# Kernel optimization log

Hardware: AMD Instinct MI355X
Metric: run time of the kernel (lower is better)

Reference implementation:

```python
import jax, jax.numpy as jnp
import numpy as np

B, H, W = 8, 80, 160
N = B * H * W          # flattened pixels
G = 8                  # cost groups
D = 64                 # disparity candidates
NS = 4                 # num_seed
E = 128                # embed_dim
NFREQ = 15             # fourier freqs -> (2*15+1)*1 = 31 dims
NORMALIZER = 3.14 / 64


def setup_inputs() -> dict:
    key = jax.random.key(0)
    ks = jax.random.split(key, 8)
    cost_volume = jax.random.normal(ks[0], (N, G, D), jnp.float32)
    label_seed = jax.random.randint(ks[1], (N, NS), 0, D)
    context = jax.random.normal(ks[2], (B, H, W, E), jnp.float32)
    s = 0.02
    W1 = jax.random.normal(ks[3], (G * 9, E), jnp.float32) * s
    b1 = jnp.zeros((E,), jnp.float32)
    W2 = jax.random.normal(ks[4], (E, E), jnp.float32) * s
    b2 = jnp.zeros((E,), jnp.float32)
    Wp = jax.random.normal(ks[5], (E + 31, E), jnp.float32) * s
    return {"cost_volume": cost_volume, "label_seed": label_seed, "context": context,
            "W1": W1, "b1": b1, "W2": W2, "b2": b2, "Wp": Wp}


def sample_cost(cost_volume, label_seed):
    # cost_volume: [N,G,D], label_seed: [N,NS] -> [N,NS,G*9]
    offset = jnp.arange(-4, 5, dtype=label_seed.dtype)              # [9]
    idx = jnp.clip(label_seed[:, :, None] + offset, 0, D - 1)      # [N,NS,9]
    idx = jnp.broadcast_to(idx.reshape(N, 1, NS * 9), (N, G, NS * 9))
    cost = jnp.take_along_axis(cost_volume, idx, axis=-1)          # [N,G,NS*9]
    # rearrange 'b h (n c) -> b n (h c)'
    cost = cost.reshape(N, G, NS, 9).transpose(0, 2, 1, 3).reshape(N, NS, G * 9)
    return cost


def fourier_embed(label_f):
    # label_f: [N,NS] float -> [N,NS,31]
    coord = label_f * NORMALIZER                                   # [N,NS]
    freqs = 2.0 ** jnp.arange(NFREQ, dtype=label_f.dtype)          # logscale bands
    f = coord[..., None] * freqs                                   # [N,NS,15]
    return jnp.concatenate([jnp.sin(f), jnp.cos(f), coord[..., None]], axis=-1)


def reference(cost_volume, label_seed, context, W1, b1, W2, b2, Wp):
    cost = sample_cost(cost_volume, label_seed)                    # [N,NS,72]
    h = jax.nn.gelu(cost @ W1 + b1, approximate=False)
    cost_feat = h @ W2 + b2                                        # [N,NS,E]
    label_f = label_seed.astype(jnp.float32)
    disp_enc = fourier_embed(label_f)                              # [N,NS,31]
    sample_embed = jnp.concatenate([cost_feat, disp_enc], axis=-1) @ Wp  # [N,NS,E]
    # layers=[] and norm=None -> passthrough; context unused
    return sample_embed[None], label_f
```

## Files before the change

kernel.cpp:

```cpp
#include <hip/hip_runtime.h>
#include <hip/hip_bf16.h>
#include <math.h>

#define NPIX 102400
#define NSEED 4
#define RTOT (NPIX * NSEED)
#define GG 8
#define DD 64
#define EE 128
#define BM 64

#define KP1 96
#define KP2 128
#define KP3 160

#define PC 104
#define PH 136
#define PF 168

typedef short bf16x8 __attribute__((ext_vector_type(8)));
typedef short bf16x4 __attribute__((ext_vector_type(4)));
typedef float f32x4 __attribute__((ext_vector_type(4)));

static __device__ __forceinline__ short f2bf(float x) {
    __hip_bfloat16 h = __float2bfloat16(x);
    return __builtin_bit_cast(short, h);
}

static __device__ __forceinline__ float gelu_exact(float x) {
    return 0.5f * x * (1.0f + erff(x * 0.7071067811865475f));
}

__global__ void prep_weights(const float* __restrict__ W1,
                             const float* __restrict__ W2,
                             const float* __restrict__ Wp,
                             short* __restrict__ ws) {
    const int i = blockIdx.x * 256 + threadIdx.x;
    if (i < 12288) {
        const int e = i / KP1, k = i - e * KP1;
        ws[i] = (k < 72) ? f2bf(W1[k * EE + e]) : (short)0;
    } else if (i < 12288 + 16384) {
        const int j = i - 12288;
        const int e = j / KP2, k = j - e * KP2;
        ws[i] = f2bf(W2[k * EE + e]);
    } else if (i < 49152) {
        const int j = i - 28672;
        const int e = j / KP3, k = j - e * KP3;
        ws[i] = (k < 159) ? f2bf(Wp[k * EE + e]) : (short)0;
    }
}

template <int KPAD, int PADB>
__device__ __forceinline__ void gemm_tiles(const short* __restrict__ WT, const short* sB,
                                           int mt0, int ln, int qd, f32x4 acc[2][4]) {
#pragma unroll
    for (int ks = 0; ks < KPAD / 32; ++ks) {
        const int kb = ks * 32 + qd * 8;
        const bf16x8 a0 = *(const bf16x8*)(WT + (mt0 * 16 + ln) * KPAD + kb);
        const bf16x8 a1 = *(const bf16x8*)(WT + (mt0 * 16 + 16 + ln) * KPAD + kb);
        const bf16x8 b0 = *(const bf16x8*)(sB + (0 * 16 + ln) * PADB + kb);
        const bf16x8 b1 = *(const bf16x8*)(sB + (1 * 16 + ln) * PADB + kb);
        const bf16x8 b2 = *(const bf16x8*)(sB + (2 * 16 + ln) * PADB + kb);
        const bf16x8 b3 = *(const bf16x8*)(sB + (3 * 16 + ln) * PADB + kb);
        acc[0][0] = __builtin_amdgcn_mfma_f32_16x16x32_bf16(a0, b0, acc[0][0], 0, 0, 0);
        acc[0][1] = __builtin_amdgcn_mfma_f32_16x16x32_bf16(a0, b1, acc[0][1], 0, 0, 0);
        acc[0][2] = __builtin_amdgcn_mfma_f32_16x16x32_bf16(a0, b2, acc[0][2], 0, 0, 0);
        acc[0][3] = __builtin_amdgcn_mfma_f32_16x16x32_bf16(a0, b3, acc[0][3], 0, 0, 0);
        acc[1][0] = __builtin_amdgcn_mfma_f32_16x16x32_bf16(a1, b0, acc[1][0], 0, 0, 0);
        acc[1][1] = __builtin_amdgcn_mfma_f32_16x16x32_bf16(a1, b1, acc[1][1], 0, 0, 0);
        acc[1][2] = __builtin_amdgcn_mfma_f32_16x16x32_bf16(a1, b2, acc[1][2], 0, 0, 0);
        acc[1][3] = __builtin_amdgcn_mfma_f32_16x16x32_bf16(a1, b3, acc[1][3], 0, 0, 0);
    }
}

__global__ __launch_bounds__(256, 4)
void Propagation_85315230368231_kernel(const float* __restrict__ cost_volume,
                                       const int* __restrict__ label_seed,
                                       const short* __restrict__ ws,
                                       const float* __restrict__ b1,
                                       const float* __restrict__ b2,
                                       float* __restrict__ out) {
    __shared__ short sU[BM * PF];
    __shared__ short sHT[BM * PH];
    __shared__ int sSeed[BM];

    const short* W1T = ws;
    const short* W2T = ws + 12288;
    const short* WpT = ws + 28672;

    const int tid = threadIdx.x;
    const int blk = blockIdx.x;
    const int p0 = blk * (BM / NSEED);
    const int row0 = blk * BM;

    const int wave = tid >> 6;
    const int lane = tid & 63;
    const int ln = lane & 15;
    const int qd = lane >> 4;
    const int mt0 = wave * 2;

    if (tid < BM) {
        const int sd = label_seed[row0 + tid];
        sSeed[tid] = sd;
        out[(size_t)RTOT * EE + row0 + tid] = (float)sd;
    }
    __syncthreads();

    for (int e = tid; e < BM * 36; e += 256) {
        const int row = e / 36;
        const int pr = e - row * 36;
        const int k0 = pr * 2, k1 = k0 + 1;
        const int sd = sSeed[row];
        const float* cvn = cost_volume + (size_t)(p0 + (row >> 2)) * (GG * DD);
        const int g0 = k0 / 9, c0 = k0 - g0 * 9;
        int d0 = sd + c0 - 4; d0 = d0 < 0 ? 0 : (d0 > 63 ? 63 : d0);
        const float v0 = cvn[g0 * DD + d0];
        const int g1 = k1 / 9, c1 = k1 - g1 * 9;
        int d1 = sd + c1 - 4; d1 = d1 < 0 ? 0 : (d1 > 63 ? 63 : d1);
        const float v1 = cvn[g1 * DD + d1];
        const int pk = (int)(unsigned short)f2bf(v0) | ((int)(unsigned short)f2bf(v1) << 16);
        *(int*)(sU + row * PC + k0) = pk;
    }
    for (int e = tid; e < BM * 12; e += 256) {
        const int row = e / 12;
        const int j = e - row * 12;
        *(int*)(sU + row * PC + 72 + 2 * j) = 0;
    }
    __syncthreads();

    f32x4 acc[2][4];

#pragma unroll
    for (int i = 0; i < 2; ++i)
#pragma unroll
        for (int j = 0; j < 4; ++j) acc[i][j] = (f32x4)0.0f;
    gemm_tiles<KP1, PC>(W1T, sU, mt0, ln, qd, acc);
#pragma unroll
    for (int mi = 0; mi < 2; ++mi) {
        const int eb = (mt0 + mi) * 16 + qd * 4;
        const float4 bv = *(const float4*)(b1 + eb);
#pragma unroll
        for (int nt = 0; nt < 4; ++nt) {
            bf16x4 p;
            p[0] = f2bf(gelu_exact(acc[mi][nt][0] + bv.x));
            p[1] = f2bf(gelu_exact(acc[mi][nt][1] + bv.y));
            p[2] = f2bf(gelu_exact(acc[mi][nt][2] + bv.z));
            p[3] = f2bf(gelu_exact(acc[mi][nt][3] + bv.w));
            *(bf16x4*)(sHT + (nt * 16 + ln) * PH + eb) = p;
        }
    }
    __syncthreads();

    for (int e = tid; e < BM * 32; e += 256) {
        const int row = e >> 5;
        const int j = e & 31;
        const float coord = (float)sSeed[row] * (float)(3.14 / 64.0);
        float v;
        if (j < 15) v = sinf(coord * (float)(1 << j));
        else if (j < 30) v = cosf(coord * (float)(1 << (j - 15)));
        else if (j == 30) v = coord;
        else v = 0.0f;
        sU[row * PF + 128 + j] = f2bf(v);
    }

#pragma unroll
    for (int i = 0; i < 2; ++i)
#pragma unroll
        for (int j = 0; j < 4; ++j) acc[i][j] = (f32x4)0.0f;
    gemm_tiles<KP2, PH>(W2T, sHT, mt0, ln, qd, acc);
#pragma unroll
    for (int mi = 0; mi < 2; ++mi) {
        const int eb = (mt0 + mi) * 16 + qd * 4;
        const float4 bv = *(const float4*)(b2 + eb);
#pragma unroll
        for (int nt = 0; nt < 4; ++nt) {
            bf16x4 p;
            p[0] = f2bf(acc[mi][nt][0] + bv.x);
            p[1] = f2bf(acc[mi][nt][1] + bv.y);
            p[2] = f2bf(acc[mi][nt][2] + bv.z);
            p[3] = f2bf(acc[mi][nt][3] + bv.w);
            *(bf16x4*)(sU + (nt * 16 + ln) * PF + eb) = p;
        }
    }
    __syncthreads();

#pragma unroll
    for (int i = 0; i < 2; ++i)
#pragma unroll
        for (int j = 0; j < 4; ++j) acc[i][j] = (f32x4)0.0f;
    gemm_tiles<KP3, PF>(WpT, sU, mt0, ln, qd, acc);
#pragma unroll
    for (int mi = 0; mi < 2; ++mi) {
        const int eb = (mt0 + mi) * 16 + qd * 4;
#pragma unroll
        for (int nt = 0; nt < 4; ++nt) {
            const size_t grow = (size_t)(row0 + nt * 16 + ln);
            float4 v = {acc[mi][nt][0], acc[mi][nt][1], acc[mi][nt][2], acc[mi][nt][3]};
            *(float4*)(out + grow * EE + eb) = v;
        }
    }
}

extern "C" void kernel_launch(void* const* d_in, const int* in_sizes, int n_in,
                              void* d_out, int out_size, void* d_ws, size_t ws_size,
                              hipStream_t stream) {
    const float* cost_volume = (const float*)d_in[0];
    const int* label_seed = (const int*)d_in[1];
    const float* W1 = (const float*)d_in[3];
    const float* b1 = (const float*)d_in[4];
    const float* W2 = (const float*)d_in[5];
    const float* b2 = (const float*)d_in[6];
    const float* Wp = (const float*)d_in[7];
    float* out = (float*)d_out;
    short* ws = (short*)d_ws;

    prep_weights<<<192, 256, 0, stream>>>(W1, W2, Wp, ws);
    Propagation_85315230368231_kernel<<<RTOT / BM, 256, 0, stream>>>(
        cost_volume, label_seed, ws, b1, b2, out);
}
```

Measured before the change: 461.3 us.

## Share one LDS buffer, table Fourier embedding, fast GELU, raise occupancy

Merges the two shared-memory tiles into a single padded buffer, adding syncs so each GEMM stage can reuse it, and raises launch bounds to 7 blocks per SM. The Fourier embedding of the seed, which depends only on an integer 0..63, is precomputed once in the weight-prep kernel and read as a small table. Exact erf-based GELU is replaced with an Abramowitz-Stegun polynomial using rcp and exp. The cost gather is restructured so each thread handles one group's 9 consecutive taps. The intent is to cut LDS footprint, transcendental math and per-row work, at the cost of extra barriers and a small loss in GELU accuracy.

New measurement: 441.4 us. -4.3%, faster.

```diff
diff --git a/kernel.cpp b/kernel.cpp
--- a/kernel.cpp
+++ b/kernel.cpp
@@ -14,9 +14,7 @@
 #define KP2 128
 #define KP3 160
 
-#define PC 104
-#define PH 136
-#define PF 168
+#define PS 168
 
 typedef short bf16x8 __attribute__((ext_vector_type(8)));
 typedef short bf16x4 __attribute__((ext_vector_type(4)));
@@ -27,8 +25,18 @@
     return __builtin_bit_cast(short, h);
 }
 
-static __device__ __forceinline__ float gelu_exact(float x) {
-    return 0.5f * x * (1.0f + erff(x * 0.7071067811865475f));
+static __device__ __forceinline__ float gelu_fast(float x) {
+    const float z = fabsf(x) * 0.7071067811865475f;
+    const float t = __builtin_amdgcn_rcpf(__builtin_fmaf(0.3275911f, z, 1.0f));
+    float p = __builtin_fmaf(1.061405429f, t, -1.453152027f);
+    p = __builtin_fmaf(p, t, 1.421413741f);
+    p = __builtin_fmaf(p, t, -0.284496736f);
+    p = __builtin_fmaf(p, t, 0.254829592f);
+    p = p * t;
+    const float e = __expf(-z * z);
+    const float q = 0.5f * p * e;
+    const float phi = (x >= 0.0f) ? (1.0f - q) : q;
+    return x * phi;
 }
 
 __global__ void prep_weights(const float* __restrict__ W1,
@@ -47,6 +55,16 @@
         const int j = i - 28672;
         const int e = j / KP3, k = j - e * KP3;
         ws[i] = (k < 159) ? f2bf(Wp[k * EE + e]) : (short)0;
+    } else if (i < 51200) {
+        const int j = i - 49152;
+        const int sd = j >> 5, c = j & 31;
+        const float coord = (float)sd * (float)(3.14 / 64.0);
+        float v;
+        if (c < 15) v = sinf(coord * (float)(1 << c));
+        else if (c < 30) v = cosf(coord * (float)(1 << (c - 15)));
+        else if (c == 30) v = coord;
+        else v = 0.0f;
+        ws[i] = f2bf(v);
     }
 }
 
@@ -73,20 +91,20 @@
     }
 }
 
-__global__ __launch_bounds__(256, 4)
+__global__ __launch_bounds__(256, 7)
 void Propagation_85315230368231_kernel(const float* __restrict__ cost_volume,
                                        const int* __restrict__ label_seed,
                                        const short* __restrict__ ws,
                                        const float* __restrict__ b1,
                                        const float* __restrict__ b2,
                                        float* __restrict__ out) {
-    __shared__ short sU[BM * PF];
-    __shared__ short sHT[BM * PH];
+    __shared__ short sU[BM * PS];
     __shared__ int sSeed[BM];
 
     const short* W1T = ws;
     const short* W2T = ws + 12288;
     const short* WpT = ws + 28672;
+    const short* Ftab = ws + 49152;
 
     const int tid = threadIdx.x;
     const int blk = blockIdx.x;
@@ -106,25 +124,36 @@
     }
     __syncthreads();
 
-    for (int e = tid; e < BM * 36; e += 256) {
-        const int row = e / 36;
-        const int pr = e - row * 36;
-        const int k0 = pr * 2, k1 = k0 + 1;
-        const int sd = sSeed[row];
-        const float* cvn = cost_volume + (size_t)(p0 + (row >> 2)) * (GG * DD);
-        const int g0 = k0 / 9, c0 = k0 - g0 * 9;
-        int d0 = sd + c0 - 4; d0 = d0 < 0 ? 0 : (d0 > 63 ? 63 : d0);
-        const float v0 = cvn[g0 * DD + d0];
-        const int g1 = k1 / 9, c1 = k1 - g1 * 9;
-        int d1 = sd + c1 - 4; d1 = d1 < 0 ? 0 : (d1 > 63 ? 63 : d1);
-        const float v1 = cvn[g1 * DD + d1];
-        const int pk = (int)(unsigned short)f2bf(v0) | ((int)(unsigned short)f2bf(v1) << 16);
-        *(int*)(sU + row * PC + k0) = pk;
-    }
-    for (int e = tid; e < BM * 12; e += 256) {
-        const int row = e / 12;
-        const int j = e - row * 12;
-        *(int*)(sU + row * PC + 72 + 2 * j) = 0;
+    {
+        const int g = tid & 7;
+#pragma unroll
+        for (int i = 0; i < 2; ++i) {
+            const int r = (tid >> 3) + i * 32;
+            const int sd = sSeed[r];
+            const float* cv = cost_volume + (size_t)(p0 + (r >> 2)) * (GG * DD) + g * DD;
+            const int dbase = sd - 4;
+            float v[9];
+#pragma unroll
+            for (int c = 0; c < 9; ++c) {
+                int d = dbase + c;
+                d = d < 0 ? 0 : d;
+                d = d > 63 ? 63 : d;
+                v[c] = cv[d];
+            }
+            short* dst = sU + r * PS + g * 9;
+#pragma unroll
+            for (int c = 0; c < 9; ++c) dst[c] = f2bf(v[c]);
+        }
+    }
+    if (tid < 192) {
+        const int r = tid / 3;
+        const int j = tid - 3 * r;
+        *(bf16x8*)(sU + r * PS + 72 + j * 8) = (bf16x8)0;
+    }
+    {
+        const int r = tid >> 2, ch = tid & 3;
+        const bf16x8 t = *(const bf16x8*)(Ftab + sSeed[r] * 32 + ch * 8);
+        *(bf16x8*)(sU + r * PS + 128 + ch * 8) = t;
     }
     __syncthreads();
 
@@ -134,7 +163,9 @@
     for (int i = 0; i < 2; ++i)
 #pragma unroll
         for (int j = 0; j < 4; ++j) acc[i][j] = (f32x4)0.0f;
-    gemm_tiles<KP1, PC>(W1T, sU, mt0, ln, qd, acc);
+    gemm_tiles<KP1, PS>(W1T, sU, mt0, ln, qd, acc);
+    __syncthreads();
+
 #pragma unroll
     for (int mi = 0; mi < 2; ++mi) {
         const int eb = (mt0 + mi) * 16 + qd * 4;
@@ -142,32 +173,22 @@
 #pragma unroll
         for (int nt = 0; nt < 4; ++nt) {
             bf16x4 p;
-            p[0] = f2bf(gelu_exact(acc[mi][nt][0] + bv.x));
-            p[1] = f2bf(gelu_exact(acc[mi][nt][1] + bv.y));
-            p[2] = f2bf(gelu_exact(acc[mi][nt][2] + bv.z));
-            p[3] = f2bf(gelu_exact(acc[mi][nt][3] + bv.w));
-            *(bf16x4*)(sHT + (nt * 16 + ln) * PH + eb) = p;
-        }
-    }
-    __syncthreads();
-
-    for (int e = tid; e < BM * 32; e += 256) {
-        const int row = e >> 5;
-        const int j = e & 31;
-        const float coord = (float)sSeed[row] * (float)(3.14 / 64.0);
-        float v;
-        if (j < 15) v = sinf(coord * (float)(1 << j));
-        else if (j < 30) v = cosf(coord * (float)(1 << (j - 15)));
-        else if (j == 30) v = coord;
-        else v = 0.0f;
-        sU[row * PF + 128 + j] = f2bf(v);
-    }
+            p[0] = f2bf(gelu_fast(acc[mi][nt][0] + bv.x));
+            p[1] = f2bf(gelu_fast(acc[mi][nt][1] + bv.y));
+            p[2] = f2bf(gelu_fast(acc[mi][nt][2] + bv.z));
+            p[3] = f2bf(gelu_fast(acc[mi][nt][3] + bv.w));
+            *(bf16x4*)(sU + (nt * 16 + ln) * PS + eb) = p;
+        }
+    }
+    __syncthreads();
 
 #pragma unroll
     for (int i = 0; i < 2; ++i)
 #pragma unroll
         for (int j = 0; j < 4; ++j) acc[i][j] = (f32x4)0.0f;
-    gemm_tiles<KP2, PH>(W2T, sHT, mt0, ln, qd, acc);
+    gemm_tiles<KP2, PS>(W2T, sU, mt0, ln, qd, acc);
+    __syncthreads();
+
 #pragma unroll
     for (int mi = 0; mi < 2; ++mi) {
         const int eb = (mt0 + mi) * 16 + qd * 4;
@@ -179,7 +200,7 @@
             p[1] = f2bf(acc[mi][nt][1] + bv.y);
             p[2] = f2bf(acc[mi][nt][2] + bv.z);
             p[3] = f2bf(acc[mi][nt][3] + bv.w);
-            *(bf16x4*)(sU + (nt * 16 + ln) * PF + eb) = p;
+            *(bf16x4*)(sU + (nt * 16 + ln) * PS + eb) = p;
         }
     }
     __syncthreads();
@@ -188,7 +209,7 @@
     for (int i = 0; i < 2; ++i)
 #pragma unroll
         for (int j = 0; j < 4; ++j) acc[i][j] = (f32x4)0.0f;
-    gemm_tiles<KP3, PF>(WpT, sU, mt0, ln, qd, acc);
+    gemm_tiles<KP3, PS>(WpT, sU, mt0, ln, qd, acc);
 #pragma unroll
     for (int mi = 0; mi < 2; ++mi) {
         const int eb = (mt0 + mi) * 16 + qd * 4;
@@ -214,7 +235,7 @@
     float* out = (float*)d_out;
     short* ws = (short*)d_ws;
 
-    prep_weights<<<192, 256, 0, stream>>>(W1, W2, Wp, ws);
+    prep_weights<<<200, 256, 0, stream>>>(W1, W2, Wp, ws);
     Propagation_85315230368231_kernel<<<RTOT / BM, 256, 0, stream>>>(
         cost_volume, label_seed, ws, b1, b2, out);
 }
```
